# Kernel optimization log

Measured on AMD Instinct MI355X. Metric: run time of the kernel, lower is better.

Reference implementation:

```python
import jax, jax.numpy as jnp
import numpy as np
from jax.scipy.special import logsumexp

TAU = 1.0
N_ITERS = 20
D = 1024
B = 65536


def setup_inputs() -> dict:
    key = jax.random.key(0)
    k1, k2 = jax.random.split(key)
    embeddings = jax.random.normal(k1, (B, D), dtype=jnp.float32)
    log_scores = jax.random.normal(k2, (D, D), dtype=jnp.float32) * 0.01
    return {"embeddings": embeddings, "log_scores": log_scores}


def _sinkhorn(log_alpha):
    # 20 alternating row/column logsumexp normalizations on a (d, d) matrix
    def body(_, la):
        la = la - logsumexp(la, axis=-1, keepdims=True)  # row normalize
        la = la - logsumexp(la, axis=-2, keepdims=True)  # col normalize
        return la
    log_alpha = jax.lax.fori_loop(0, N_ITERS, body, log_alpha)
    return jnp.exp(log_alpha)


def reference(embeddings, log_scores):
    P = _sinkhorn(log_scores / TAU)           # (d, d) approx doubly stochastic
    # (P @ embeddings.T).T == embeddings @ P.T
    return embeddings @ P.T                   # (B, d)
```

## Files before the change

### kernel.cpp

```cpp
#include <hip/hip_runtime.h>
#include <hip/hip_bf16.h>

#define D_DIM 1024
#define NITER 20

typedef float f32x4 __attribute__((ext_vector_type(4)));
typedef __bf16 bf16x4 __attribute__((ext_vector_type(4)));
typedef __bf16 bf16x8 __attribute__((ext_vector_type(8)));

__global__ __launch_bounds__(1024)
void prep_exp_transpose(const float* __restrict__ ls, float* __restrict__ Mm,
                        float* __restrict__ Mt, float* __restrict__ u) {
    __shared__ float tile[64][65];
    const int tx = threadIdx.x, ty = threadIdx.y;
    const int bx = blockIdx.x * 64, by = blockIdx.y * 64;
#pragma unroll
    for (int k = 0; k < 64; k += 16) {
        int r = by + ty + k, c = bx + tx;
        float v = expf(ls[r * D_DIM + c]);
        Mm[r * D_DIM + c] = v;
        tile[ty + k][tx] = v;
    }
    if (blockIdx.x == 0 && blockIdx.y == 0) u[ty * 64 + tx] = 1.0f;
    __syncthreads();
#pragma unroll
    for (int k = 0; k < 64; k += 16) {
        int r = bx + ty + k, c = by + tx;
        Mt[r * D_DIM + c] = tile[tx][ty + k];
    }
}

__global__ __launch_bounds__(256)
void matvec_recip(const float* __restrict__ A, const float* __restrict__ x,
                  float* __restrict__ y) {
    const int wave = threadIdx.x >> 6, lane = threadIdx.x & 63;
    const int row = blockIdx.x * 4 + wave;
    const f32x4* Ar = (const f32x4*)(A + row * D_DIM);
    const f32x4* xr = (const f32x4*)x;
    float s = 0.f;
#pragma unroll
    for (int it = 0; it < 4; ++it) {
        f32x4 a = Ar[lane + it * 64];
        f32x4 b = xr[lane + it * 64];
        s += a.x * b.x + a.y * b.y + a.z * b.z + a.w * b.w;
    }
#pragma unroll
    for (int off = 32; off > 0; off >>= 1) s += __shfl_down(s, off, 64);
    if (lane == 0) y[row] = 1.0f / s;
}

__global__ __launch_bounds__(256)
void finalize_P(const float* __restrict__ Mm, const float* __restrict__ r,
                const float* __restrict__ u, __bf16* __restrict__ P) {
    const int i = blockIdx.x;
    const int t = threadIdx.x;
    const float ri = r[i];
    f32x4 m = ((const f32x4*)(Mm + i * D_DIM))[t];
    f32x4 uu = ((const f32x4*)u)[t];
    bf16x4 o;
    o[0] = (__bf16)(m.x * ri * uu.x);
    o[1] = (__bf16)(m.y * ri * uu.y);
    o[2] = (__bf16)(m.z * ri * uu.z);
    o[3] = (__bf16)(m.w * ri * uu.w);
    ((bf16x4*)(P + i * D_DIM))[t] = o;
}

#define BM 128
#define BN 128
#define BK 32

__global__ __launch_bounds__(256)
void gemm_a32_bt16(const float* __restrict__ A, const __bf16* __restrict__ Bt,
                   float* __restrict__ C, int Msz, int Nsz, int Ksz) {
    __shared__ __bf16 As[BM * BK];
    __shared__ __bf16 Bs[BN * BK];
    const int tid = threadIdx.x;
    const int wave = tid >> 6, lane = tid & 63;
    const int wm = wave >> 1, wn = wave & 1;
    const int quad = lane >> 4, l16 = lane & 15;
    const int f = blockIdx.x;
    const int xcd = f & 7, s = f >> 3;
    const int m0 = (((s >> 3) << 3) | xcd) * BM;
    const int n0 = (s & 7) * BN;
    const int sR = (l16 >> 1) & 3;

    f32x4 acc[4][4] = {};

    for (int k0 = 0; k0 < Ksz; k0 += BK) {
        __syncthreads();
#pragma unroll
        for (int itc = 0; itc < 4; ++itc) {
            int idx = tid + itc * 256;
            int arow = idx >> 3, kq = idx & 7;
            f32x4 v = *(const f32x4*)(A + (size_t)(m0 + arow) * Ksz + k0 + kq * 4);
            bf16x4 b;
            b[0] = (__bf16)v.x; b[1] = (__bf16)v.y;
            b[2] = (__bf16)v.z; b[3] = (__bf16)v.w;
            int slot = (kq >> 1) ^ ((arow >> 1) & 3);
            *(bf16x4*)(&As[arow * BK + slot * 8 + (kq & 1) * 4]) = b;
        }
#pragma unroll
        for (int q = 0; q < 2; ++q) {
            int t8 = wave * 2 + q;
            int nrow = t8 * 16 + (lane >> 2);
            int kb = (lane & 3) ^ ((lane >> 3) & 3);
            const __bf16* g = Bt + (size_t)(n0 + nrow) * Ksz + k0 + kb * 8;
            __bf16* l = Bs + t8 * 512;
            __builtin_amdgcn_global_load_lds(
                (const __attribute__((address_space(1))) void*)g,
                (__attribute__((address_space(3))) void*)l, 16, 0, 0);
        }
        __syncthreads();

        bf16x8 af[4], bfr[4];
#pragma unroll
        for (int a = 0; a < 4; ++a) {
            int arow = wm * 64 + a * 16 + l16;
            af[a] = *(const bf16x8*)(&As[arow * BK + (quad ^ sR) * 8]);
        }
#pragma unroll
        for (int b = 0; b < 4; ++b) {
            int brow = wn * 64 + b * 16 + l16;
            bfr[b] = *(const bf16x8*)(&Bs[brow * BK + (quad ^ sR) * 8]);
        }
#pragma unroll
        for (int a = 0; a < 4; ++a)
#pragma unroll
            for (int b = 0; b < 4; ++b)
                acc[a][b] = __builtin_amdgcn_mfma_f32_16x16x32_bf16(
                    af[a], bfr[b], acc[a][b], 0, 0, 0);
    }

#pragma unroll
    for (int a = 0; a < 4; ++a) {
        int mg = m0 + wm * 64 + a * 16 + quad * 4;
#pragma unroll
        for (int b = 0; b < 4; ++b) {
            int ng = n0 + wn * 64 + b * 16 + l16;
#pragma unroll
            for (int v = 0; v < 4; ++v)
                C[(size_t)(mg + v) * Nsz + ng] = acc[a][b][v];
        }
    }
}

extern "C" void kernel_launch(void* const* d_in, const int* in_sizes, int n_in,
                              void* d_out, int out_size, void* d_ws, size_t ws_size,
                              hipStream_t stream) {
    const float* emb = (const float*)d_in[0];
    const float* ls  = (const float*)d_in[1];
    float* out = (float*)d_out;
    char* ws = (char*)d_ws;

    float* Mm  = (float*)ws;
    float* Mt  = (float*)(ws + (4u << 20));
    float* r   = (float*)(ws + (8u << 20));
    float* u   = (float*)(ws + (8u << 20) + 4096);
    __bf16* P  = (__bf16*)(ws + (8u << 20) + 8192);

    const int B = in_sizes[0] / D_DIM;

    prep_exp_transpose<<<dim3(16, 16), dim3(64, 16), 0, stream>>>(ls, Mm, Mt, u);
    for (int it = 0; it < NITER; ++it) {
        matvec_recip<<<D_DIM / 4, 256, 0, stream>>>(Mm, u, r);
        matvec_recip<<<D_DIM / 4, 256, 0, stream>>>(Mt, r, u);
    }
    finalize_P<<<D_DIM, 256, 0, stream>>>(Mm, r, u, P);
    gemm_a32_bt16<<<dim3((B / BM) * (D_DIM / BN)), 256, 0, stream>>>(
        emb, P, out, B, D_DIM, D_DIM);
}
```

Measured before the change: 709.5 us.

## Fuse Sinkhorn iterations into one cooperative kernel and pre-convert embeddings to bf16

Result: slower. 814.1 us (+14.8%).

```diff
diff --git a/kernel.cpp b/kernel.cpp
--- a/kernel.cpp
+++ b/kernel.cpp
@@ -3,6 +3,7 @@
 
 #define D_DIM 1024
 #define NITER 20
+#define NBLK 32
 
 typedef float f32x4 __attribute__((ext_vector_type(4)));
 typedef __bf16 bf16x4 __attribute__((ext_vector_type(4)));
@@ -10,7 +11,8 @@
 
 __global__ __launch_bounds__(1024)
 void prep_exp_transpose(const float* __restrict__ ls, float* __restrict__ Mm,
-                        float* __restrict__ Mt, float* __restrict__ u) {
+                        float* __restrict__ Mt, float* __restrict__ u,
+                        unsigned* __restrict__ cnt) {
     __shared__ float tile[64][65];
     const int tx = threadIdx.x, ty = threadIdx.y;
     const int bx = blockIdx.x * 64, by = blockIdx.y * 64;
@@ -21,7 +23,10 @@
         Mm[r * D_DIM + c] = v;
         tile[ty + k][tx] = v;
     }
-    if (blockIdx.x == 0 && blockIdx.y == 0) u[ty * 64 + tx] = 1.0f;
+    if (blockIdx.x == 0 && blockIdx.y == 0) {
+        u[ty * 64 + tx] = 1.0f;
+        if (tx == 0 && ty == 0) *cnt = 0u;
+    }
     __syncthreads();
 #pragma unroll
     for (int k = 0; k < 64; k += 16) {
@@ -30,23 +35,86 @@
     }
 }
 
-__global__ __launch_bounds__(256)
-void matvec_recip(const float* __restrict__ A, const float* __restrict__ x,
-                  float* __restrict__ y) {
-    const int wave = threadIdx.x >> 6, lane = threadIdx.x & 63;
-    const int row = blockIdx.x * 4 + wave;
-    const f32x4* Ar = (const f32x4*)(A + row * D_DIM);
-    const f32x4* xr = (const f32x4*)x;
-    float s = 0.f;
-#pragma unroll
-    for (int it = 0; it < 4; ++it) {
-        f32x4 a = Ar[lane + it * 64];
-        f32x4 b = xr[lane + it * 64];
-        s += a.x * b.x + a.y * b.y + a.z * b.z + a.w * b.w;
-    }
-#pragma unroll
-    for (int off = 32; off > 0; off >>= 1) s += __shfl_down(s, off, 64);
-    if (lane == 0) y[row] = 1.0f / s;
+__device__ inline void gbar(unsigned* cnt, unsigned& target) {
+    __syncthreads();
+    if (threadIdx.x == 0) {
+        __threadfence();
+        __hip_atomic_fetch_add(cnt, 1u, __ATOMIC_ACQ_REL, __HIP_MEMORY_SCOPE_AGENT);
+        target += NBLK;
+        while (__hip_atomic_load(cnt, __ATOMIC_ACQUIRE, __HIP_MEMORY_SCOPE_AGENT) < target)
+            __builtin_amdgcn_s_sleep(2);
+        __threadfence();
+    }
+    __syncthreads();
+}
+
+__global__ __launch_bounds__(1024)
+void sinkhorn_iters(const float* __restrict__ Mm, const float* __restrict__ Mt,
+                    float* __restrict__ r, float* __restrict__ u,
+                    unsigned* __restrict__ cnt) {
+    __shared__ float vec[D_DIM];
+    const int tid = threadIdx.x;
+    const int wid = tid >> 6, lane = tid & 63;
+    const int row0 = blockIdx.x * 32 + wid * 2;
+
+    const f32x4* A0 = (const f32x4*)(Mm + (size_t)row0 * D_DIM);
+    const f32x4* A1 = (const f32x4*)(Mm + (size_t)(row0 + 1) * D_DIM);
+    const f32x4* T0 = (const f32x4*)(Mt + (size_t)row0 * D_DIM);
+    const f32x4* T1 = (const f32x4*)(Mt + (size_t)(row0 + 1) * D_DIM);
+    f32x4 a0[4], a1[4], t0[4], t1[4];
+#pragma unroll
+    for (int q = 0; q < 4; ++q) {
+        a0[q] = A0[lane + q * 64]; a1[q] = A1[lane + q * 64];
+        t0[q] = T0[lane + q * 64]; t1[q] = T1[lane + q * 64];
+    }
+
+    vec[tid] = u[tid];
+    __syncthreads();
+
+    unsigned target = 0;
+    for (int it = 0; it < NITER; ++it) {
+        float s0 = 0.f, s1 = 0.f;
+#pragma unroll
+        for (int q = 0; q < 4; ++q) {
+            f32x4 b = ((const f32x4*)vec)[lane + q * 64];
+            s0 += a0[q].x * b.x + a0[q].y * b.y + a0[q].z * b.z + a0[q].w * b.w;
+            s1 += a1[q].x * b.x + a1[q].y * b.y + a1[q].z * b.z + a1[q].w * b.w;
+        }
+#pragma unroll
+        for (int off = 32; off; off >>= 1) {
+            s0 += __shfl_down(s0, off, 64);
+            s1 += __shfl_down(s1, off, 64);
+        }
+        if (lane == 0) {
+            __hip_atomic_store(&r[row0], 1.0f / s0, __ATOMIC_RELAXED, __HIP_MEMORY_SCOPE_AGENT);
+            __hip_atomic_store(&r[row0 + 1], 1.0f / s1, __ATOMIC_RELAXED, __HIP_MEMORY_SCOPE_AGENT);
+        }
+        gbar(cnt, target);
+        vec[tid] = __hip_atomic_load(&r[tid], __ATOMIC_RELAXED, __HIP_MEMORY_SCOPE_AGENT);
+        __syncthreads();
+
+        s0 = 0.f; s1 = 0.f;
+#pragma unroll
+        for (int q = 0; q < 4; ++q) {
+            f32x4 b = ((const f32x4*)vec)[lane + q * 64];
+            s0 += t0[q].x * b.x + t0[q].y * b.y + t0[q].z * b.z + t0[q].w * b.w;
+            s1 += t1[q].x * b.x + t1[q].y * b.y + t1[q].z * b.z + t1[q].w * b.w;
+        }
+#pragma unroll
+        for (int off = 32; off; off >>= 1) {
+            s0 += __shfl_down(s0, off, 64);
+            s1 += __shfl_down(s1, off, 64);
+        }
+        if (lane == 0) {
+            __hip_atomic_store(&u[row0], 1.0f / s0, __ATOMIC_RELAXED, __HIP_MEMORY_SCOPE_AGENT);
+            __hip_atomic_store(&u[row0 + 1], 1.0f / s1, __ATOMIC_RELAXED, __HIP_MEMORY_SCOPE_AGENT);
+        }
+        if (it < NITER - 1) {
+            gbar(cnt, target);
+            vec[tid] = __hip_atomic_load(&u[tid], __ATOMIC_RELAXED, __HIP_MEMORY_SCOPE_AGENT);
+            __syncthreads();
+        }
+    }
 }
 
 __global__ __launch_bounds__(256)
@@ -65,9 +133,89 @@
     ((bf16x4*)(P + i * D_DIM))[t] = o;
 }
 
+__global__ __launch_bounds__(256)
+void convert_bf16(const float* __restrict__ A, __bf16* __restrict__ Ab, long n8) {
+    const long stride = (long)gridDim.x * 256;
+    for (long i = (long)blockIdx.x * 256 + threadIdx.x; i < n8; i += stride) {
+        f32x4 v0 = ((const f32x4*)A)[2 * i];
+        f32x4 v1 = ((const f32x4*)A)[2 * i + 1];
+        bf16x8 o;
+        o[0] = (__bf16)v0.x; o[1] = (__bf16)v0.y; o[2] = (__bf16)v0.z; o[3] = (__bf16)v0.w;
+        o[4] = (__bf16)v1.x; o[5] = (__bf16)v1.y; o[6] = (__bf16)v1.z; o[7] = (__bf16)v1.w;
+        ((bf16x8*)Ab)[i] = o;
+    }
+}
+
 #define BM 128
 #define BN 128
 #define BK 32
+
+__global__ __launch_bounds__(256)
+void gemm_bt16(const __bf16* __restrict__ A, const __bf16* __restrict__ Bt,
+               float* __restrict__ C, int Msz, int Nsz, int Ksz) {
+    __shared__ __bf16 As[BM * BK];
+    __shared__ __bf16 Bs[BN * BK];
+    const int tid = threadIdx.x;
+    const int wave = tid >> 6, lane = tid & 63;
+    const int wm = wave >> 1, wn = wave & 1;
+    const int quad = lane >> 4, l16 = lane & 15;
+    const int f = blockIdx.x;
+    const int xcd = f & 7, s = f >> 3;
+    const int m0 = (((s >> 3) << 3) | xcd) * BM;
+    const int n0 = (s & 7) * BN;
+    const int sR = (l16 >> 1) & 3;
+
+    f32x4 acc[4][4] = {};
+
+    for (int k0 = 0; k0 < Ksz; k0 += BK) {
+        __syncthreads();
+#pragma unroll
+        for (int q = 0; q < 2; ++q) {
+            int t8 = wave * 2 + q;
+            int row = t8 * 16 + (lane >> 2);
+            int kb = (lane & 3) ^ ((lane >> 3) & 3);
+            const __bf16* ga = A + (size_t)(m0 + row) * Ksz + k0 + kb * 8;
+            __builtin_amdgcn_global_load_lds(
+                (const __attribute__((address_space(1))) void*)ga,
+                (__attribute__((address_space(3))) void*)(As + t8 * 512), 16, 0, 0);
+            const __bf16* gb = Bt + (size_t)(n0 + row) * Ksz + k0 + kb * 8;
+            __builtin_amdgcn_global_load_lds(
+                (const __attribute__((address_space(1))) void*)gb,
+                (__attribute__((address_space(3))) void*)(Bs + t8 * 512), 16, 0, 0);
+        }
+        __syncthreads();
+
+        bf16x8 af[4], bfr[4];
+#pragma unroll
+        for (int a = 0; a < 4; ++a) {
+            int arow = wm * 64 + a * 16 + l16;
+            af[a] = *(const bf16x8*)(&As[arow * BK + (quad ^ sR) * 8]);
+        }
+#pragma unroll
+        for (int b = 0; b < 4; ++b) {
+            int brow = wn * 64 + b * 16 + l16;
+            bfr[b] = *(const bf16x8*)(&Bs[brow * BK + (quad ^ sR) * 8]);
+        }
+#pragma unroll
+        for (int a = 0; a < 4; ++a)
+#pragma unroll
+            for (int b = 0; b < 4; ++b)
+                acc[a][b] = __builtin_amdgcn_mfma_f32_16x16x32_bf16(
+                    af[a], bfr[b], acc[a][b], 0, 0, 0);
+    }
+
+#pragma unroll
+    for (int a = 0; a < 4; ++a) {
+        int mg = m0 + wm * 64 + a * 16 + quad * 4;
+#pragma unroll
+        for (int b = 0; b < 4; ++b) {
+            int ng = n0 + wn * 64 + b * 16 + l16;
+#pragma unroll
+            for (int v = 0; v < 4; ++v)
+                C[(size_t)(mg + v) * Nsz + ng] = acc[a][b][v];
+        }
+    }
+}
 
 __global__ __launch_bounds__(256)
 void gemm_a32_bt16(const float* __restrict__ A, const __bf16* __restrict__ Bt,
@@ -105,10 +253,9 @@
             int nrow = t8 * 16 + (lane >> 2);
             int kb = (lane & 3) ^ ((lane >> 3) & 3);
             const __bf16* g = Bt + (size_t)(n0 + nrow) * Ksz + k0 + kb * 8;
-            __bf16* l = Bs + t8 * 512;
             __builtin_amdgcn_global_load_lds(
                 (const __attribute__((address_space(1))) void*)g,
-                (__attribute__((address_space(3))) void*)l, 16, 0, 0);
+                (__attribute__((address_space(3))) void*)(Bs + t8 * 512), 16, 0, 0);
         }
         __syncthreads();
 
@@ -152,20 +299,34 @@
     float* out = (float*)d_out;
     char* ws = (char*)d_ws;
 
-    float* Mm  = (float*)ws;
-    float* Mt  = (float*)(ws + (4u << 20));
-    float* r   = (float*)(ws + (8u << 20));
-    float* u   = (float*)(ws + (8u << 20) + 4096);
-    __bf16* P  = (__bf16*)(ws + (8u << 20) + 8192);
-
-    const int B = in_sizes[0] / D_DIM;
-
-    prep_exp_transpose<<<dim3(16, 16), dim3(64, 16), 0, stream>>>(ls, Mm, Mt, u);
-    for (int it = 0; it < NITER; ++it) {
-        matvec_recip<<<D_DIM / 4, 256, 0, stream>>>(Mm, u, r);
-        matvec_recip<<<D_DIM / 4, 256, 0, stream>>>(Mt, r, u);
-    }
+    float* Mm     = (float*)ws;
+    float* Mt     = (float*)(ws + (4u << 20));
+    float* r      = (float*)(ws + (8u << 20));
+    float* u      = (float*)(ws + (8u << 20) + 4096);
+    unsigned* cnt = (unsigned*)(ws + (8u << 20) + 8192);
+    __bf16* P     = (__bf16*)(ws + (8u << 20) + 12288);
+    __bf16* Ab    = (__bf16*)(ws + (16u << 20));
+
+    const int Bv = in_sizes[0] / D_DIM;
+    const size_t need = (16u << 20) + (size_t)Bv * D_DIM * sizeof(__bf16);
+
+    prep_exp_transpose<<<dim3(16, 16), dim3(64, 16), 0, stream>>>(ls, Mm, Mt, u, cnt);
+
+    void* cargs[5];
+    cargs[0] = (void*)&Mm; cargs[1] = (void*)&Mt;
+    cargs[2] = (void*)&r;  cargs[3] = (void*)&u;
+    cargs[4] = (void*)&cnt;
+    hipLaunchCooperativeKernel(sinkhorn_iters, dim3(NBLK), dim3(1024), cargs, 0,
+                               stream);
+
     finalize_P<<<D_DIM, 256, 0, stream>>>(Mm, r, u, P);
-    gemm_a32_bt16<<<dim3((B / BM) * (D_DIM / BN)), 256, 0, stream>>>(
-        emb, P, out, B, D_DIM, D_DIM);
-}
+
+    if (ws_size >= need) {
+        convert_bf16<<<2048, 256, 0, stream>>>(emb, Ab, (long)Bv * D_DIM / 8);
+        gemm_bt16<<<dim3((Bv / BM) * (D_DIM / BN)), 256, 0, stream>>>(
+            Ab, P, out, Bv, D_DIM, D_DIM);
+    } else {
+        gemm_a32_bt16<<<dim3((Bv / BM) * (D_DIM / BN)), 256, 0, stream>>>(
+            emb, P, out, Bv, D_DIM, D_DIM);
+    }
+}
```
